# Kernel optimization log

Hardware: AMD Instinct MI355X
Metric: run time of the kernel (lower is better)

The kernel has to match this reference:

```python
import jax, jax.numpy as jnp
import numpy as np

BS, NA, NE, NAL = 512, 8, 8, 7        # batch, agents, enemies, allies
OWN_F, EN_F, AL_F = 16, 16, 16        # per-entity feature dims
H, HEADS, HYPER, OUT_N = 64, 4, 64, 6 # rnn_hidden_dim, hpn heads, hyper hidden, normal actions
D_E = (EN_F * H + H + 1) * HEADS      # hypernet-enemy out: input-layer W + fc2 W + fc2 b (per head)
D_A = AL_F * H * HEADS                # hypernet-ally out: input-layer W only (non-MMM map)


def setup_inputs() -> dict:
    key = jax.random.key(0)
    ks = jax.random.split(key, 16)
    def w(k, shape, fan):
        return jax.random.normal(k, shape, jnp.float32) / np.sqrt(fan)
    n = BS * NA
    return dict(
        own_feats=jax.random.normal(ks[0], (n, OWN_F), jnp.float32),
        enemy_feats=jax.random.normal(ks[1], (n * NE, EN_F), jnp.float32),
        ally_feats=jax.random.normal(ks[2], (n * NAL, AL_F), jnp.float32),
        hidden_state=jax.random.normal(ks[3], (n, H), jnp.float32),
        fc1_w=w(ks[4], (OWN_F, H), OWN_F), fc1_b=jnp.zeros((H,), jnp.float32),
        he_w1=w(ks[5], (EN_F, HYPER), EN_F), he_b1=jnp.zeros((HYPER,), jnp.float32),
        he_w2=w(ks[6], (HYPER, D_E), HYPER), he_b2=jnp.zeros((D_E,), jnp.float32),
        ha_w1=w(ks[7], (AL_F, HYPER), AL_F), ha_b1=jnp.zeros((HYPER,), jnp.float32),
        ha_w2=w(ks[8], (HYPER, D_A), HYPER), ha_b2=jnp.zeros((D_A,), jnp.float32),
        w_in_merge=jnp.full((HEADS, H), 1.0 / HEADS, jnp.float32),
        gru_w_ih=w(ks[9], (3 * H, H), H), gru_b_ih=jnp.zeros((3 * H,), jnp.float32),
        gru_w_hh=w(ks[10], (3 * H, H), H), gru_b_hh=jnp.zeros((3 * H,), jnp.float32),
        fc2_w=w(ks[11], (H, OUT_N), H), fc2_b=jnp.zeros((OUT_N,), jnp.float32),
        w_out_merge=jnp.full((HEADS,), 1.0 / HEADS, jnp.float32),
    )


def reference(own_feats, enemy_feats, ally_feats, hidden_state,
              fc1_w, fc1_b, he_w1, he_b1, he_w2, he_b2,
              ha_w1, ha_b1, ha_w2, ha_b2, w_in_merge,
              gru_w_ih, gru_b_ih, gru_w_hh, gru_b_hh,
              fc2_w, fc2_b, w_out_merge):
    n = own_feats.shape[0]  # bs * n_agents
    # --- hypernetworks (per-entity MLPs generating weights) ---
    hyper_e = jax.nn.relu(enemy_feats @ he_w1 + he_b1) @ he_w2 + he_b2  # (n*NE, D_E)
    hyper_a = jax.nn.relu(ally_feats @ ha_w1 + ha_b1) @ ha_w2 + ha_b2   # (n*NAL, D_A)
    # --- permutation-invariant input embedding: generated input weights, sum over entities ---
    w1_e = hyper_e[:, :EN_F * H * HEADS].reshape(n, NE, EN_F, H, HEADS)
    emb_e = jnp.einsum('nef,nefhk->nhk', enemy_feats.reshape(n, NE, EN_F), w1_e)
    w1_a = hyper_a.reshape(n, NAL, AL_F, H, HEADS)
    emb_a = jnp.einsum('naf,nafhk->nhk', ally_feats.reshape(n, NAL, AL_F), w1_a)
    merged = jnp.einsum('nhk,kh->nh', emb_e + emb_a, w_in_merge)  # Merger over heads
    embedding = own_feats @ fc1_w + fc1_b + merged
    x = jax.nn.relu(embedding)
    # --- GRUCell (torch semantics) ---
    gi = x @ gru_w_ih.T + gru_b_ih
    gh = hidden_state @ gru_w_hh.T + gru_b_hh
    ir, iz, ig = jnp.split(gi, 3, axis=-1)
    hr, hz, hg = jnp.split(gh, 3, axis=-1)
    r = jax.nn.sigmoid(ir + hr)
    z = jax.nn.sigmoid(iz + hz)
    g = jnp.tanh(ig + r * hg)
    hh = (1.0 - z) * g + z * hidden_state  # (n, H)
    # --- normal-action Q head ---
    q_normal = (hh @ fc2_w + fc2_b).reshape(BS, NA, OUT_N)
    # --- attack Q: generated per-enemy fc2 weights/bias, tiny batched GEMV + head merge ---
    w2 = hyper_e[:, -(H + 1) * HEADS:-HEADS].reshape(n, NE, H, HEADS)
    b2 = hyper_e[:, -HEADS:].reshape(n, NE, HEADS)
    q_attacks = jnp.einsum('nh,nehk->nek', hh, w2) + b2  # (n, NE, HEADS)
    q_attack = (q_attacks @ w_out_merge).reshape(BS, NA, NE)  # unify_output_heads
    q = jnp.concatenate([q_normal, q_attack], axis=-1)
    return q.reshape(BS, NA, -1), hh.reshape(BS, NA, H)
```

## Files before the change

### kernel.cpp

```cpp
#include <hip/hip_runtime.h>
#include <math.h>

#define NAGT 4096
#define NE 8
#define NAL 7
#define QTOT (NAGT*14)
#define D_E 4356
#define D_A 4096
#define KPAD 2112

#define WBIG_OFF 0
#define WBIG_SZ (KPAD*64)
#define WIHT_OFF (WBIG_OFF + WBIG_SZ)
#define WIHT_SZ (64*192)
#define WHHT_OFF (WIHT_OFF + WIHT_SZ)
#define WATT_OFF (WHHT_OFF + WIHT_SZ)
#define WATTB_OFF (WATT_OFF + 4096)
#define BATTT_OFF (WATTB_OFF + 64)
#define BATT0_OFF (BATTT_OFF + 64)

#define PREP_ITEMS (WBIG_SZ + 2*WIHT_SZ + 4096 + 64 + 64 + 1)
#define PREP_BLOCKS ((PREP_ITEMS + 255)/256)

__device__ __forceinline__ float dot4w(const float* __restrict__ p,
                                       const float* __restrict__ wim, int h) {
    return p[0]*wim[h] + p[1]*wim[64+h] + p[2]*wim[128+h] + p[3]*wim[192+h];
}

__global__ __launch_bounds__(256) void k_prep(
    const float* __restrict__ hew2, const float* __restrict__ heb2,
    const float* __restrict__ haw2, const float* __restrict__ hab2,
    const float* __restrict__ wim,  const float* __restrict__ wih,
    const float* __restrict__ whh,  const float* __restrict__ wom,
    const float* __restrict__ fc1w, float* __restrict__ ws)
{
    int idx = blockIdx.x*256 + threadIdx.x;
    if (idx >= PREP_ITEMS) return;
    if (idx < WBIG_SZ) {
        int rr = idx >> 6, h = idx & 63;
        float s;
        if (rr < 1024) {
            int f = rr >> 6, j = rr & 63;
            s = dot4w(hew2 + (size_t)j*D_E + f*256 + h*4, wim, h);
        } else if (rr < 2048) {
            int r2 = rr - 1024; int f = r2 >> 6, j = r2 & 63;
            s = dot4w(haw2 + (size_t)j*D_A + f*256 + h*4, wim, h);
        } else if (rr < 2064) {
            s = dot4w(heb2 + (rr - 2048)*256 + h*4, wim, h);
        } else if (rr < 2080) {
            s = dot4w(hab2 + (rr - 2064)*256 + h*4, wim, h);
        } else if (rr < 2096) {
            s = fc1w[(rr - 2080)*64 + h];
        } else {
            s = 0.f;
        }
        ws[WBIG_OFF + idx] = s;
        return;
    }
    int k2 = idx - WBIG_SZ;
    if (k2 < WIHT_SZ) {
        int h = k2 / 192, c = k2 % 192;
        ws[WIHT_OFF + k2] = wih[c*64 + h];
        return;
    }
    k2 -= WIHT_SZ;
    if (k2 < WIHT_SZ) {
        int h = k2 / 192, c = k2 % 192;
        ws[WHHT_OFF + k2] = whh[c*64 + h];
        return;
    }
    k2 -= WIHT_SZ;
    if (k2 < 4096) {
        int h = k2 >> 6, j = k2 & 63;
        float s = 0.f;
        #pragma unroll
        for (int k = 0; k < 4; k++)
            s = fmaf(wom[k], hew2[(size_t)j*D_E + 4096 + h*4 + k], s);
        ws[WATT_OFF + k2] = s;
        return;
    }
    k2 -= 4096;
    if (k2 < 64) {
        int j = k2;
        float s = 0.f;
        #pragma unroll
        for (int k = 0; k < 4; k++)
            s = fmaf(wom[k], hew2[(size_t)j*D_E + 4352 + k], s);
        ws[WATTB_OFF + j] = s;
        return;
    }
    k2 -= 64;
    if (k2 < 64) {
        int h = k2;
        float s = 0.f;
        #pragma unroll
        for (int k = 0; k < 4; k++)
            s = fmaf(wom[k], heb2[4096 + h*4 + k], s);
        ws[BATTT_OFF + h] = s;
        return;
    }
    {
        float s = 0.f;
        #pragma unroll
        for (int k = 0; k < 4; k++) s = fmaf(wom[k], heb2[4352 + k], s);
        ws[BATT0_OFF] = s;
    }
}

struct SM {
    float relu_e[8][8][64];
    float relu_a[8][7][64];
    float ef_l[8][8][16];
    float af_l[8][7][16];
    float tails[8][64];
    float pa_lds[4][8][64];
    float embp[4][8][64];
    float lH[8][64];
    float lHH[8][64];
    float lU[8][64];
};

__global__ __launch_bounds__(256) void k_fused(
    const float* __restrict__ own,  const float* __restrict__ ef,
    const float* __restrict__ af,   const float* __restrict__ hidden,
    const float* __restrict__ fc1b, const float* __restrict__ heb1,
    const float* __restrict__ hew1, const float* __restrict__ hab1,
    const float* __restrict__ haw1, const float* __restrict__ gbih,
    const float* __restrict__ gbhh, const float* __restrict__ fc2w,
    const float* __restrict__ fc2b, const float* __restrict__ ws,
    float* __restrict__ out)
{
    __shared__ SM sm;
    int bid = blockIdx.x, t = threadIdx.x;
    int w = t >> 6, l = t & 63;
    int n0 = bid * 8;

    ((float4*)sm.ef_l)[t] = ((const float4*)(ef + (size_t)n0*128))[t];
    if (t < 224) ((float4*)sm.af_l)[t] = ((const float4*)(af + (size_t)n0*112))[t];
    if (t < 128) {
        int a = t >> 4, f = t & 15;
        sm.tails[a][32+f] = own[(size_t)n0*16 + t];
        sm.tails[a][48+f] = 0.f;
        ((float4*)sm.lH)[t] = ((const float4*)(hidden + (size_t)n0*64))[t];
    }
    __syncthreads();

    for (int i = 0; i < 30; i++) {
        int r = w*30 + i;
        int a = r / 15, ent = r % 15;
        if (ent < 8) {
            float accv = heb1[l];
            #pragma unroll
            for (int f = 0; f < 16; f++)
                accv = fmaf(sm.ef_l[a][ent][f], hew1[f*64 + l], accv);
            sm.relu_e[a][ent][l] = fmaxf(accv, 0.f);
        } else {
            int al = ent - 8;
            float accv = hab1[l];
            #pragma unroll
            for (int f = 0; f < 16; f++)
                accv = fmaf(sm.af_l[a][al][f], haw1[f*64 + l], accv);
            sm.relu_a[a][al][l] = fmaxf(accv, 0.f);
        }
    }
    if (t < 128) {
        int a = t >> 4, f = t & 15;
        float se = 0.f, sa = 0.f;
        #pragma unroll
        for (int e = 0; e < 8; e++) se += sm.ef_l[a][e][f];
        #pragma unroll
        for (int e = 0; e < 7; e++) sa += sm.af_l[a][e][f];
        sm.tails[a][f] = se;
        sm.tails[a][16+f] = sa;
    }
    __syncthreads();

    float acc[8];
    #pragma unroll
    for (int a = 0; a < 8; a++) acc[a] = 0.f;
    const float* Wb = ws + WBIG_OFF;
    for (int rr = w; rr < 33; rr += 4) {
        #pragma unroll 2
        for (int a = 0; a < 8; a++) {
            float pa;
            if (rr < 16) {
                pa = 0.f;
                #pragma unroll
                for (int e = 0; e < 8; e++)
                    pa = fmaf(sm.ef_l[a][e][rr], sm.relu_e[a][e][l], pa);
            } else if (rr < 32) {
                pa = 0.f;
                #pragma unroll
                for (int e = 0; e < 7; e++)
                    pa = fmaf(sm.af_l[a][e][rr-16], sm.relu_a[a][e][l], pa);
            } else {
                pa = sm.tails[a][l];
            }
            sm.pa_lds[w][a][l] = pa;
        }
        const float* wbase = Wb + rr*4096 + l;
        #pragma unroll 4
        for (int k4 = 0; k4 < 16; k4++) {
            float wb0 = wbase[(k4*4+0)*64];
            float wb1 = wbase[(k4*4+1)*64];
            float wb2 = wbase[(k4*4+2)*64];
            float wb3 = wbase[(k4*4+3)*64];
            #pragma unroll
            for (int a = 0; a < 8; a++) {
                float4 pa4 = *(const float4*)&sm.pa_lds[w][a][k4*4];
                acc[a] = fmaf(pa4.x, wb0, acc[a]);
                acc[a] = fmaf(pa4.y, wb1, acc[a]);
                acc[a] = fmaf(pa4.z, wb2, acc[a]);
                acc[a] = fmaf(pa4.w, wb3, acc[a]);
            }
        }
    }
    #pragma unroll
    for (int a = 0; a < 8; a++) sm.embp[w][a][l] = acc[a];
    __syncthreads();

    #pragma unroll
    for (int ii = 0; ii < 2; ii++) {
        int idx = t + ii*256;
        int a = idx >> 6, h = idx & 63;
        float emb = fc1b[h];
        #pragma unroll
        for (int sw = 0; sw < 4; sw++) emb += sm.embp[sw][a][h];
        sm.embp[0][a][h] = fmaxf(emb, 0.f);
    }
    __syncthreads();

    {
        int a0 = w*2;
        float hid[2], gir[2], giz[2], gig[2], ghr[2], ghz[2], ghg[2];
        #pragma unroll
        for (int q = 0; q < 2; q++) {
            hid[q] = sm.lH[a0+q][l];
            gir[q] = gbih[l]; giz[q] = gbih[64+l]; gig[q] = gbih[128+l];
            ghr[q] = gbhh[l]; ghz[q] = gbhh[64+l]; ghg[q] = gbhh[128+l];
        }
        const float* WihT = ws + WIHT_OFF;
        const float* WhhT = ws + WHHT_OFF;
        #pragma unroll 8
        for (int h = 0; h < 64; h++) {
            float wri = WihT[h*192 + l], wzi = WihT[h*192 + 64 + l], wgi = WihT[h*192 + 128 + l];
            float wrh = WhhT[h*192 + l], wzh = WhhT[h*192 + 64 + l], wgh = WhhT[h*192 + 128 + l];
            #pragma unroll
            for (int q = 0; q < 2; q++) {
                float xv = sm.embp[0][a0+q][h], hv = sm.lH[a0+q][h];
                gir[q] = fmaf(xv, wri, gir[q]); giz[q] = fmaf(xv, wzi, giz[q]);
                gig[q] = fmaf(xv, wgi, gig[q]);
                ghr[q] = fmaf(hv, wrh, ghr[q]); ghz[q] = fmaf(hv, wzh, ghz[q]);
                ghg[q] = fmaf(hv, wgh, ghg[q]);
            }
        }
        #pragma unroll
        for (int q = 0; q < 2; q++) {
            float r = 1.f/(1.f + expf(-(gir[q] + ghr[q])));
            float z = 1.f/(1.f + expf(-(giz[q] + ghz[q])));
            float g = tanhf(gig[q] + r*ghg[q]);
            float hv = (1.f - z)*g + z*hid[q];
            sm.lHH[a0+q][l] = hv;
            out[QTOT + (size_t)(n0 + a0 + q)*64 + l] = hv;
        }

        const float* WattT = ws + WATT_OFF;
        float b0 = ws[BATT0_OFF];
        float u[2], cb[2];
        #pragma unroll
        for (int q = 0; q < 2; q++) { u[q] = ws[WATTB_OFF + l]; cb[q] = b0; }
        #pragma unroll 8
        for (int h = 0; h < 64; h++) {
            float wa = WattT[h*64 + l];
            float bt = ws[BATTT_OFF + h];
            #pragma unroll
            for (int q = 0; q < 2; q++) {
                float hv = sm.lHH[a0+q][h];
                u[q]  = fmaf(hv, wa, u[q]);
                cb[q] = fmaf(hv, bt, cb[q]);
            }
        }
        #pragma unroll
        for (int q = 0; q < 2; q++) sm.lU[a0+q][l] = u[q];

        int e = l >> 3, p = l & 7;
        #pragma unroll
        for (int q = 0; q < 2; q++) {
            int a = a0 + q, n = n0 + a;
            float4 r0 = *(const float4*)&sm.relu_e[a][e][p*8];
            float4 r1 = *(const float4*)&sm.relu_e[a][e][p*8 + 4];
            float s = 0.f;
            s = fmaf(r0.x, sm.lU[a][p*8 + 0], s); s = fmaf(r0.y, sm.lU[a][p*8 + 1], s);
            s = fmaf(r0.z, sm.lU[a][p*8 + 2], s); s = fmaf(r0.w, sm.lU[a][p*8 + 3], s);
            s = fmaf(r1.x, sm.lU[a][p*8 + 4], s); s = fmaf(r1.y, sm.lU[a][p*8 + 5], s);
            s = fmaf(r1.z, sm.lU[a][p*8 + 6], s); s = fmaf(r1.w, sm.lU[a][p*8 + 7], s);
            s += __shfl_xor(s, 1); s += __shfl_xor(s, 2); s += __shfl_xor(s, 4);
            if (p == 0) out[(size_t)n*14 + 6 + e] = s + cb[q];
        }
        if (l < 12) {
            int q = l / 6, o = l % 6;
            float qn = fc2b[o];
            #pragma unroll 8
            for (int h = 0; h < 64; h++) qn = fmaf(sm.lHH[a0+q][h], fc2w[h*6 + o], qn);
            out[(size_t)(n0 + a0 + q)*14 + o] = qn;
        }
    }
}

extern "C" void kernel_launch(void* const* d_in, const int* in_sizes, int n_in,
                              void* d_out, int out_size, void* d_ws, size_t ws_size,
                              hipStream_t stream) {
    const float* own   = (const float*)d_in[0];
    const float* ef    = (const float*)d_in[1];
    const float* af    = (const float*)d_in[2];
    const float* hidden= (const float*)d_in[3];
    const float* fc1w  = (const float*)d_in[4];
    const float* fc1b  = (const float*)d_in[5];
    const float* hew1  = (const float*)d_in[6];
    const float* heb1  = (const float*)d_in[7];
    const float* hew2  = (const float*)d_in[8];
    const float* heb2  = (const float*)d_in[9];
    const float* haw1  = (const float*)d_in[10];
    const float* hab1  = (const float*)d_in[11];
    const float* haw2  = (const float*)d_in[12];
    const float* hab2  = (const float*)d_in[13];
    const float* wim   = (const float*)d_in[14];
    const float* wih   = (const float*)d_in[15];
    const float* gbih  = (const float*)d_in[16];
    const float* whh   = (const float*)d_in[17];
    const float* gbhh  = (const float*)d_in[18];
    const float* fc2w  = (const float*)d_in[19];
    const float* fc2b  = (const float*)d_in[20];
    const float* wom   = (const float*)d_in[21];
    float* out = (float*)d_out;
    float* ws  = (float*)d_ws;

    k_prep<<<PREP_BLOCKS, 256, 0, stream>>>(hew2, heb2, haw2, hab2, wim,
                                            wih, whh, wom, fc1w, ws);
    k_fused<<<NAGT/8, 256, 0, stream>>>(own, ef, af, hidden, fc1b, heb1,
                                        hew1, hab1, haw1, gbih, gbhh,
                                        fc2w, fc2b, ws, out);
}
```

Before: 174.4 us.

## Use 512-thread blocks with register-tiled float4 weight GEMM and LDS union

Doubles the block to 8 waves so the 33 K-row groups are split across 8 waves instead of 4. Each lane now computes a 4-output by 8-agent tile using float4 weight loads, with a cross-lane shuffle reduction over K groups, replacing the scalar-load inner product. LDS is trimmed by overlaying the ally relu buffer with epilogue scratch, and the merged partial-sum buffer is used to support higher occupancy. The GRU/epilogue runs on only half the waves, which leaves the other waves idle during that phase.

Measured after the change: 145.4 us. 1.2x faster.

```diff
diff --git a/kernel.cpp b/kernel.cpp
--- a/kernel.cpp
+++ b/kernel.cpp
@@ -107,20 +107,20 @@
     }
 }
 
-struct SM {
+struct SMT {
     float relu_e[8][8][64];
-    float relu_a[8][7][64];
+    union {
+        float relu_a[8][7][64];
+        struct { float lHH[8][64]; float lU[8][64]; } ep;
+    } u;
     float ef_l[8][8][16];
     float af_l[8][7][16];
     float tails[8][64];
-    float pa_lds[4][8][64];
-    float embp[4][8][64];
+    float pamem[8][8][64];
     float lH[8][64];
-    float lHH[8][64];
-    float lU[8][64];
 };
 
-__global__ __launch_bounds__(256) void k_fused(
+__global__ __launch_bounds__(512, 4) void k_fused(
     const float* __restrict__ own,  const float* __restrict__ ef,
     const float* __restrict__ af,   const float* __restrict__ hidden,
     const float* __restrict__ fc1b, const float* __restrict__ heb1,
@@ -130,12 +130,12 @@
     const float* __restrict__ fc2b, const float* __restrict__ ws,
     float* __restrict__ out)
 {
-    __shared__ SM sm;
+    __shared__ SMT sm;
     int bid = blockIdx.x, t = threadIdx.x;
     int w = t >> 6, l = t & 63;
     int n0 = bid * 8;
 
-    ((float4*)sm.ef_l)[t] = ((const float4*)(ef + (size_t)n0*128))[t];
+    if (t < 256) ((float4*)sm.ef_l)[t] = ((const float4*)(ef + (size_t)n0*128))[t];
     if (t < 224) ((float4*)sm.af_l)[t] = ((const float4*)(af + (size_t)n0*112))[t];
     if (t < 128) {
         int a = t >> 4, f = t & 15;
@@ -145,22 +145,20 @@
     }
     __syncthreads();
 
-    for (int i = 0; i < 30; i++) {
-        int r = w*30 + i;
-        int a = r / 15, ent = r % 15;
+    for (int ent = 0; ent < 15; ent++) {
         if (ent < 8) {
             float accv = heb1[l];
             #pragma unroll
             for (int f = 0; f < 16; f++)
-                accv = fmaf(sm.ef_l[a][ent][f], hew1[f*64 + l], accv);
-            sm.relu_e[a][ent][l] = fmaxf(accv, 0.f);
+                accv = fmaf(sm.ef_l[w][ent][f], hew1[f*64 + l], accv);
+            sm.relu_e[w][ent][l] = fmaxf(accv, 0.f);
         } else {
             int al = ent - 8;
             float accv = hab1[l];
             #pragma unroll
             for (int f = 0; f < 16; f++)
-                accv = fmaf(sm.af_l[a][al][f], haw1[f*64 + l], accv);
-            sm.relu_a[a][al][l] = fmaxf(accv, 0.f);
+                accv = fmaf(sm.af_l[w][al][f], haw1[f*64 + l], accv);
+            sm.u.relu_a[w][al][l] = fmaxf(accv, 0.f);
         }
     }
     if (t < 128) {
@@ -175,12 +173,16 @@
     }
     __syncthreads();
 
-    float acc[8];
+    int kg = l >> 4, hp = l & 15;
+    float acc[8][4];
     #pragma unroll
-    for (int a = 0; a < 8; a++) acc[a] = 0.f;
+    for (int a = 0; a < 8; a++)
+        #pragma unroll
+        for (int c = 0; c < 4; c++) acc[a][c] = 0.f;
     const float* Wb = ws + WBIG_OFF;
-    for (int rr = w; rr < 33; rr += 4) {
-        #pragma unroll 2
+
+    for (int rr = w; rr < 33; rr += 8) {
+        #pragma unroll
         for (int a = 0; a < 8; a++) {
             float pa;
             if (rr < 16) {
@@ -192,45 +194,56 @@
                 pa = 0.f;
                 #pragma unroll
                 for (int e = 0; e < 7; e++)
-                    pa = fmaf(sm.af_l[a][e][rr-16], sm.relu_a[a][e][l], pa);
+                    pa = fmaf(sm.af_l[a][e][rr-16], sm.u.relu_a[a][e][l], pa);
             } else {
                 pa = sm.tails[a][l];
             }
-            sm.pa_lds[w][a][l] = pa;
-        }
-        const float* wbase = Wb + rr*4096 + l;
-        #pragma unroll 4
-        for (int k4 = 0; k4 < 16; k4++) {
-            float wb0 = wbase[(k4*4+0)*64];
-            float wb1 = wbase[(k4*4+1)*64];
-            float wb2 = wbase[(k4*4+2)*64];
-            float wb3 = wbase[(k4*4+3)*64];
-            #pragma unroll
-            for (int a = 0; a < 8; a++) {
-                float4 pa4 = *(const float4*)&sm.pa_lds[w][a][k4*4];
-                acc[a] = fmaf(pa4.x, wb0, acc[a]);
-                acc[a] = fmaf(pa4.y, wb1, acc[a]);
-                acc[a] = fmaf(pa4.z, wb2, acc[a]);
-                acc[a] = fmaf(pa4.w, wb3, acc[a]);
+            sm.pamem[w][a][l] = pa;
+        }
+        const float* wbase = Wb + rr*4096 + kg*1024 + hp*4;
+        #pragma unroll
+        for (int kk4 = 0; kk4 < 4; kk4++) {
+            float4 pa4[8];
+            #pragma unroll
+            for (int a = 0; a < 8; a++)
+                pa4[a] = *(const float4*)&sm.pamem[w][a][kg*16 + kk4*4];
+            #pragma unroll
+            for (int uu = 0; uu < 4; uu++) {
+                float4 wv = *(const float4*)(wbase + (kk4*4 + uu)*64);
+                #pragma unroll
+                for (int a = 0; a < 8; a++) {
+                    float p = (uu==0) ? pa4[a].x : (uu==1) ? pa4[a].y
+                             : (uu==2) ? pa4[a].z : pa4[a].w;
+                    acc[a][0] = fmaf(p, wv.x, acc[a][0]);
+                    acc[a][1] = fmaf(p, wv.y, acc[a][1]);
+                    acc[a][2] = fmaf(p, wv.z, acc[a][2]);
+                    acc[a][3] = fmaf(p, wv.w, acc[a][3]);
+                }
             }
         }
     }
     #pragma unroll
-    for (int a = 0; a < 8; a++) sm.embp[w][a][l] = acc[a];
+    for (int a = 0; a < 8; a++) {
+        float v0 = acc[a][0], v1 = acc[a][1], v2 = acc[a][2], v3 = acc[a][3];
+        v0 += __shfl_xor(v0, 16); v0 += __shfl_xor(v0, 32);
+        v1 += __shfl_xor(v1, 16); v1 += __shfl_xor(v1, 32);
+        v2 += __shfl_xor(v2, 16); v2 += __shfl_xor(v2, 32);
+        v3 += __shfl_xor(v3, 16); v3 += __shfl_xor(v3, 32);
+        float vv = (kg==0) ? v0 : (kg==1) ? v1 : (kg==2) ? v2 : v3;
+        sm.pamem[w][a][4*hp + kg] = vv;
+    }
     __syncthreads();
 
-    #pragma unroll
-    for (int ii = 0; ii < 2; ii++) {
-        int idx = t + ii*256;
-        int a = idx >> 6, h = idx & 63;
+    {
+        int a = t >> 6, h = t & 63;
         float emb = fc1b[h];
         #pragma unroll
-        for (int sw = 0; sw < 4; sw++) emb += sm.embp[sw][a][h];
-        sm.embp[0][a][h] = fmaxf(emb, 0.f);
+        for (int sw = 0; sw < 8; sw++) emb += sm.pamem[sw][a][h];
+        sm.pamem[0][a][h] = fmaxf(emb, 0.f);
     }
     __syncthreads();
 
-    {
+    if (w < 4) {
         int a0 = w*2;
         float hid[2], gir[2], giz[2], gig[2], ghr[2], ghz[2], ghg[2];
         #pragma unroll
@@ -247,7 +260,7 @@
             float wrh = WhhT[h*192 + l], wzh = WhhT[h*192 + 64 + l], wgh = WhhT[h*192 + 128 + l];
             #pragma unroll
             for (int q = 0; q < 2; q++) {
-                float xv = sm.embp[0][a0+q][h], hv = sm.lH[a0+q][h];
+                float xv = sm.pamem[0][a0+q][h], hv = sm.lH[a0+q][h];
                 gir[q] = fmaf(xv, wri, gir[q]); giz[q] = fmaf(xv, wzi, giz[q]);
                 gig[q] = fmaf(xv, wgi, gig[q]);
                 ghr[q] = fmaf(hv, wrh, ghr[q]); ghz[q] = fmaf(hv, wzh, ghz[q]);
@@ -260,28 +273,28 @@
             float z = 1.f/(1.f + expf(-(giz[q] + ghz[q])));
             float g = tanhf(gig[q] + r*ghg[q]);
             float hv = (1.f - z)*g + z*hid[q];
-            sm.lHH[a0+q][l] = hv;
+            sm.u.ep.lHH[a0+q][l] = hv;
             out[QTOT + (size_t)(n0 + a0 + q)*64 + l] = hv;
         }
 
         const float* WattT = ws + WATT_OFF;
         float b0 = ws[BATT0_OFF];
-        float u[2], cb[2];
-        #pragma unroll
-        for (int q = 0; q < 2; q++) { u[q] = ws[WATTB_OFF + l]; cb[q] = b0; }
+        float uacc[2], cb[2];
+        #pragma unroll
+        for (int q = 0; q < 2; q++) { uacc[q] = ws[WATTB_OFF + l]; cb[q] = b0; }
         #pragma unroll 8
         for (int h = 0; h < 64; h++) {
             float wa = WattT[h*64 + l];
             float bt = ws[BATTT_OFF + h];
             #pragma unroll
             for (int q = 0; q < 2; q++) {
-                float hv = sm.lHH[a0+q][h];
-                u[q]  = fmaf(hv, wa, u[q]);
-                cb[q] = fmaf(hv, bt, cb[q]);
+                float hv = sm.u.ep.lHH[a0+q][h];
+                uacc[q] = fmaf(hv, wa, uacc[q]);
+                cb[q]   = fmaf(hv, bt, cb[q]);
             }
         }
         #pragma unroll
-        for (int q = 0; q < 2; q++) sm.lU[a0+q][l] = u[q];
+        for (int q = 0; q < 2; q++) sm.u.ep.lU[a0+q][l] = uacc[q];
 
         int e = l >> 3, p = l & 7;
         #pragma unroll
@@ -290,10 +303,10 @@
             float4 r0 = *(const float4*)&sm.relu_e[a][e][p*8];
             float4 r1 = *(const float4*)&sm.relu_e[a][e][p*8 + 4];
             float s = 0.f;
-            s = fmaf(r0.x, sm.lU[a][p*8 + 0], s); s = fmaf(r0.y, sm.lU[a][p*8 + 1], s);
-            s = fmaf(r0.z, sm.lU[a][p*8 + 2], s); s = fmaf(r0.w, sm.lU[a][p*8 + 3], s);
-            s = fmaf(r1.x, sm.lU[a][p*8 + 4], s); s = fmaf(r1.y, sm.lU[a][p*8 + 5], s);
-            s = fmaf(r1.z, sm.lU[a][p*8 + 6], s); s = fmaf(r1.w, sm.lU[a][p*8 + 7], s);
+            s = fmaf(r0.x, sm.u.ep.lU[a][p*8 + 0], s); s = fmaf(r0.y, sm.u.ep.lU[a][p*8 + 1], s);
+            s = fmaf(r0.z, sm.u.ep.lU[a][p*8 + 2], s); s = fmaf(r0.w, sm.u.ep.lU[a][p*8 + 3], s);
+            s = fmaf(r1.x, sm.u.ep.lU[a][p*8 + 4], s); s = fmaf(r1.y, sm.u.ep.lU[a][p*8 + 5], s);
+            s = fmaf(r1.z, sm.u.ep.lU[a][p*8 + 6], s); s = fmaf(r1.w, sm.u.ep.lU[a][p*8 + 7], s);
             s += __shfl_xor(s, 1); s += __shfl_xor(s, 2); s += __shfl_xor(s, 4);
             if (p == 0) out[(size_t)n*14 + 6 + e] = s + cb[q];
         }
@@ -301,7 +314,7 @@
             int q = l / 6, o = l % 6;
             float qn = fc2b[o];
             #pragma unroll 8
-            for (int h = 0; h < 64; h++) qn = fmaf(sm.lHH[a0+q][h], fc2w[h*6 + o], qn);
+            for (int h = 0; h < 64; h++) qn = fmaf(sm.u.ep.lHH[a0+q][h], fc2w[h*6 + o], qn);
             out[(size_t)(n0 + a0 + q)*14 + o] = qn;
         }
     }
@@ -337,7 +350,7 @@
 
     k_prep<<<PREP_BLOCKS, 256, 0, stream>>>(hew2, heb2, haw2, hab2, wim,
                                             wih, whh, wom, fc1w, ws);
-    k_fused<<<NAGT/8, 256, 0, stream>>>(own, ef, af, hidden, fc1b, heb1,
+    k_fused<<<NAGT/8, 512, 0, stream>>>(own, ef, af, hidden, fc1b, heb1,
                                         hew1, hab1, haw1, gbih, gbhh,
                                         fc2w, fc2b, ws, out);
 }
```
